# Kernel tuning notes

Hardware: AMD Instinct MI355X
Metric: run time of the kernel (lower is better)

## Reference

```python
import jax, jax.numpy as jnp
import numpy as np

B, S, D = 4, 2048, 1024

def setup_inputs() -> dict:
    key = jax.random.key(0)
    ks = jax.random.split(key, 4)
    scale = 1.0 / np.sqrt(D)
    return {
        "x": jax.random.normal(ks[0], (B, S, D), dtype=jnp.float32),
        "Wq": jax.random.normal(ks[1], (D, D), dtype=jnp.float32) * scale,
        "bq": jnp.zeros((D,), dtype=jnp.float32),
        "Wk": jax.random.normal(ks[2], (D, D), dtype=jnp.float32) * scale,
        "bk": jnp.zeros((D,), dtype=jnp.float32),
        "Wv": jax.random.normal(ks[3], (D, D), dtype=jnp.float32) * scale,
        "bv": jnp.zeros((D,), dtype=jnp.float32),
    }

def reference(x, Wq, bq, Wk, bk, Wv, bv):
    d = x.shape[-1]
    Q = jnp.einsum('bsd,df->bsf', x, Wq) + bq  # [B,S,D]
    K = jnp.einsum('bsd,df->bsf', x, Wk) + bk
    V = jnp.einsum('bsd,df->bsf', x, Wv) + bv
    scores = jnp.einsum('bqd,bkd->bqk', Q, K) / jnp.sqrt(jnp.asarray(d, x.dtype))  # [B,S,S]
    weights = jax.nn.softmax(scores, axis=-1)
    return jnp.einsum('bqk,bkd->bqd', weights, V)  # [B,S,D]
```

## Files before the change

kernel.cpp:

```cpp
#include <hip/hip_runtime.h>
#include <stdint.h>


typedef __attribute__((ext_vector_type(8))) short bf16x8;
typedef __attribute__((ext_vector_type(4))) float f32x4;
typedef __attribute__((ext_vector_type(4))) unsigned short u16x4;
typedef __attribute__((ext_vector_type(8))) unsigned short u16x8;

__device__ __forceinline__ unsigned short f2bf(float f) {
  union { float f; unsigned u; } v; v.f = f;
  return (unsigned short)((v.u + 0x7FFFu + ((v.u >> 16) & 1u)) >> 16);
}
__device__ __forceinline__ unsigned short f2h(float f) {
  union { _Float16 h; unsigned short u; } v; v.h = (_Float16)f;
  return v.u;
}
__device__ __forceinline__ float h2f(unsigned short u) {
  union { unsigned short u; _Float16 h; } v; v.u = u;
  return (float)v.h;
}

__device__ __forceinline__ void gload16(const void* g, void* l) {
  __builtin_amdgcn_global_load_lds(
      (const __attribute__((address_space(1))) unsigned int*)g,
      (__attribute__((address_space(3))) unsigned int*)l, 16, 0, 0);
}

template <int N>
__device__ __forceinline__ void wait_vm() {
  asm volatile("s_waitcnt vmcnt(%0)" ::"n"(N) : "memory");
}

__device__ __forceinline__ int swz8(int bid, int cpx) {
  return (bid & 7) * cpx + (bid >> 3);
}

__device__ __forceinline__ f32x4 mfma16(bf16x8 a, bf16x8 b, f32x4 c) {
  return __builtin_amdgcn_mfma_f32_16x16x32_bf16(a, b, c, 0, 0, 0);
}

__device__ __forceinline__ void gemm_core(
    const unsigned short* __restrict__ A, const unsigned short* __restrict__ Bt,
    const int lda, const int ldb, const int nt,
    const long aRow0, const long bRow0, char* lds,
    f32x4 (&acc)[8][4]) {
  constexpr int A_BYTES = 256 * 64;
  constexpr int SLOT = A_BYTES + 128 * 64;
  constexpr int LA = 4, LB = 2, L = LA + LB;
  const int tid = threadIdx.x;
  const int lane = tid & 63;
  const int wid = tid >> 6;
  const int wm = wid >> 1, wn = wid & 1;
  const int l15 = lane & 15, lhi = lane >> 4;

  long goffA[LA]; int ldsoffA[LA];
#pragma unroll
  for (int j = 0; j < LA; ++j) {
    const int local = j * 4096 + tid * 16;
    const int row = local >> 6, ch = (local >> 4) & 3;
    goffA[j] = (aRow0 + row) * (long)lda + ((ch ^ ((row >> 1) & 3)) << 3);
    ldsoffA[j] = local;
  }
  long goffB[LB]; int ldsoffB[LB];
#pragma unroll
  for (int j = 0; j < LB; ++j) {
    const int local = j * 4096 + tid * 16;
    const int row = local >> 6, ch = (local >> 4) & 3;
    goffB[j] = (bRow0 + row) * (long)ldb + ((ch ^ ((row >> 1) & 3)) << 3);
    ldsoffB[j] = A_BYTES + local;
  }
  int raddrA[8];
#pragma unroll
  for (int m = 0; m < 8; ++m) {
    const int row = wm * 128 + m * 16 + l15;
    raddrA[m] = row * 64 + ((lhi ^ ((row >> 1) & 3)) << 4);
  }
  int raddrB[4];
#pragma unroll
  for (int n = 0; n < 4; ++n) {
    const int row = wn * 64 + n * 16 + l15;
    raddrB[n] = A_BYTES + row * 64 + ((lhi ^ ((row >> 1) & 3)) << 4);
  }

  const f32x4 z4 = {0.f, 0.f, 0.f, 0.f};
#pragma unroll
  for (int m = 0; m < 8; ++m)
#pragma unroll
    for (int n = 0; n < 4; ++n) acc[m][n] = z4;

  auto stage_tile = [&](int T) {
    char* dst = lds + (T % 3) * SLOT;
    const int k0 = T << 5;
#pragma unroll
    for (int j = 0; j < LA; ++j) gload16(A + goffA[j] + k0, dst + ldsoffA[j]);
#pragma unroll
    for (int j = 0; j < LB; ++j) gload16(Bt + goffB[j] + k0, dst + ldsoffB[j]);
  };

  stage_tile(0);
  stage_tile(1);
  wait_vm<L>();
  __builtin_amdgcn_s_barrier();

  for (int t = 0; t < nt; ++t) {
    const char* sb = lds + (t % 3) * SLOT;
    bf16x8 af[8], bfr[4];
#pragma unroll
    for (int n = 0; n < 4; ++n) bfr[n] = *(const bf16x8*)(sb + raddrB[n]);
#pragma unroll
    for (int m = 0; m < 8; ++m) af[m] = *(const bf16x8*)(sb + raddrA[m]);
    if (t + 2 < nt) stage_tile(t + 2);
    __builtin_amdgcn_s_setprio(1);
#pragma unroll
    for (int m = 0; m < 8; ++m)
#pragma unroll
      for (int n = 0; n < 4; ++n) acc[m][n] = mfma16(af[m], bfr[n], acc[m][n]);
    __builtin_amdgcn_s_setprio(0);
    if (t + 2 < nt) wait_vm<L>();
    else if (t + 1 < nt) wait_vm<0>();
    __builtin_amdgcn_s_barrier();
  }
}

__global__ __launch_bounds__(256, 2) void qkv_kernel(
    const unsigned short* __restrict__ X, const unsigned short* __restrict__ TQ,
    const unsigned short* __restrict__ TK, const unsigned short* __restrict__ TV,
    const float* __restrict__ bq, const float* __restrict__ bk,
    const float* __restrict__ bv, unsigned short* __restrict__ Q16,
    unsigned short* __restrict__ K16, unsigned short* __restrict__ VT) {
  __shared__ char lds[3 * 24576];
  const int wgid = swz8(blockIdx.x, 96);
  const int tm = wgid / 24, tn = wgid % 24;
  const int w = tn >> 3, c = tn & 7;
  const unsigned short* Bt = w == 0 ? TQ : (w == 1 ? TK : TV);
  const float* bias = w == 0 ? bq : (w == 1 ? bk : bv);

  f32x4 acc[8][4];
  gemm_core(X, Bt, 1024, 1024, 32, (long)tm * 256, (long)c * 128, lds, acc);

  const int tid = threadIdx.x, lane = tid & 63, wid = tid >> 6;
  const int wm = wid >> 1, wn = wid & 1;
  const int l15 = lane & 15, lhi = lane >> 4;
  const int rowBase = tm * 256 + wm * 128;
  const int colBase = c * 128 + wn * 64;
  if (w < 2) {
    unsigned short* C = w == 0 ? Q16 : K16;
#pragma unroll
    for (int m = 0; m < 8; ++m)
#pragma unroll
      for (int n = 0; n < 4; ++n) {
        const int col = colBase + n * 16 + l15;
        const float bvv = bias[col];
#pragma unroll
        for (int j = 0; j < 4; ++j) {
          const int row = rowBase + m * 16 + lhi * 4 + j;
          C[(long)row * 1024 + col] = f2bf(acc[m][n][j] + bvv);
        }
      }
  } else {
#pragma unroll
    for (int m = 0; m < 8; ++m)
#pragma unroll
      for (int n = 0; n < 4; ++n) {
        const int col = colBase + n * 16 + l15;
        const float bvv = bias[col];
        const int row0 = rowBase + m * 16 + lhi * 4;
        const int b = row0 >> 11, s = row0 & 2047;
        u16x4 v;
#pragma unroll
        for (int j = 0; j < 4; ++j) v[j] = f2bf(acc[m][n][j] + bvv);
        *reinterpret_cast<u16x4*>(&VT[(long)b * 2097152 + (long)col * 2048 + s]) = v;
      }
  }
}

__global__ __launch_bounds__(256, 2) void scores_kernel(
    const unsigned short* __restrict__ Q16, const unsigned short* __restrict__ K16,
    unsigned short* __restrict__ SC16) {
  __shared__ char lds[3 * 24576];
  const int wgid = swz8(blockIdx.x, 64);
  const int bz = wgid >> 7, tm = (wgid >> 4) & 7, tn = wgid & 15;
  const unsigned short* A = Q16 + (long)bz * 2097152;
  const unsigned short* Bt = K16 + (long)bz * 2097152;

  f32x4 acc[8][4];
  gemm_core(A, Bt, 1024, 1024, 32, (long)tm * 256, (long)tn * 128, lds, acc);

  unsigned short* C = SC16 + (long)bz * 4194304;
  const int tid = threadIdx.x, lane = tid & 63, wid = tid >> 6;
  const int wm = wid >> 1, wn = wid & 1;
  const int l15 = lane & 15, lhi = lane >> 4;
  const int rowBase = tm * 256 + wm * 128;
  const int colBase = tn * 128 + wn * 64;
#pragma unroll
  for (int m = 0; m < 8; ++m)
#pragma unroll
    for (int n = 0; n < 4; ++n) {
      const int col = colBase + n * 16 + l15;
#pragma unroll
      for (int j = 0; j < 4; ++j) {
        const int row = rowBase + m * 16 + lhi * 4 + j;
        C[(long)row * 2048 + col] = f2h(acc[m][n][j] * (1.f / 32.f));
      }
    }
}

__global__ __launch_bounds__(256, 2) void pv_kernel(
    const unsigned short* __restrict__ P16, const unsigned short* __restrict__ VT,
    float* __restrict__ out) {
  __shared__ char lds[3 * 24576];
  const int wgid = swz8(blockIdx.x, 32);
  const int bz = wgid >> 6, tm = (wgid >> 3) & 7, tn = wgid & 7;
  const unsigned short* A = P16 + (long)bz * 4194304;
  const unsigned short* Bt = VT + (long)bz * 2097152;

  f32x4 acc[8][4];
  gemm_core(A, Bt, 2048, 2048, 64, (long)tm * 256, (long)tn * 128, lds, acc);

  float* C = out + (long)bz * 2097152;
  const int tid = threadIdx.x, lane = tid & 63, wid = tid >> 6;
  const int wm = wid >> 1, wn = wid & 1;
  const int l15 = lane & 15, lhi = lane >> 4;
  const int rowBase = tm * 256 + wm * 128;
  const int colBase = tn * 128 + wn * 64;
#pragma unroll
  for (int m = 0; m < 8; ++m)
#pragma unroll
    for (int n = 0; n < 4; ++n) {
      const int col = colBase + n * 16 + l15;
#pragma unroll
      for (int j = 0; j < 4; ++j) {
        const int row = rowBase + m * 16 + lhi * 4 + j;
        C[(long)row * 1024 + col] = acc[m][n][j];
      }
    }
}

__global__ __launch_bounds__(256) void cvt4(const float* __restrict__ in,
                                            unsigned short* __restrict__ out) {
  int i = blockIdx.x * 256 + threadIdx.x;
  float4 v = reinterpret_cast<const float4*>(in)[i];
  u16x4 r;
  r[0] = f2bf(v.x); r[1] = f2bf(v.y); r[2] = f2bf(v.z); r[3] = f2bf(v.w);
  reinterpret_cast<u16x4*>(out)[i] = r;
}

__global__ __launch_bounds__(256) void cvtWt(
    const float* __restrict__ w0, const float* __restrict__ w1, const float* __restrict__ w2,
    unsigned short* __restrict__ t0, unsigned short* __restrict__ t1, unsigned short* __restrict__ t2) {
  const float* w = blockIdx.y == 0 ? w0 : (blockIdx.y == 1 ? w1 : w2);
  unsigned short* t = blockIdx.y == 0 ? t0 : (blockIdx.y == 1 ? t1 : t2);
  int id = blockIdx.x * 256 + threadIdx.x;
  int k = id >> 10, n = id & 1023;
  t[n * 1024 + k] = f2bf(w[id]);
}

__global__ __launch_bounds__(256) void softmax_rows(const unsigned short* __restrict__ S,
                                                    unsigned short* __restrict__ P) {
  const long row = blockIdx.x;
  const u16x8* src = reinterpret_cast<const u16x8*>(S + row * 2048);
  const int tid = threadIdx.x;
  u16x8 a = src[tid];
  float v[8];
#pragma unroll
  for (int i = 0; i < 8; ++i) v[i] = h2f(a[i]);
  float m = v[0];
#pragma unroll
  for (int i = 1; i < 8; ++i) m = fmaxf(m, v[i]);
#pragma unroll
  for (int o = 32; o > 0; o >>= 1) m = fmaxf(m, __shfl_xor(m, o));
  __shared__ float red[8];
  const int wid = tid >> 6, lane = tid & 63;
  if (lane == 0) red[wid] = m;
  __syncthreads();
  m = fmaxf(fmaxf(red[0], red[1]), fmaxf(red[2], red[3]));
  float s = 0.f;
#pragma unroll
  for (int i = 0; i < 8; ++i) { v[i] = __expf(v[i] - m); s += v[i]; }
#pragma unroll
  for (int o = 32; o > 0; o >>= 1) s += __shfl_xor(s, o);
  if (lane == 0) red[4 + wid] = s;
  __syncthreads();
  s = (red[4] + red[5]) + (red[6] + red[7]);
  const float inv = 1.f / s;
  u16x8 p;
#pragma unroll
  for (int i = 0; i < 8; ++i) p[i] = f2bf(v[i] * inv);
  reinterpret_cast<u16x8*>(P + row * 2048)[tid] = p;
}

extern "C" void kernel_launch(void* const* d_in, const int* in_sizes, int n_in,
                              void* d_out, int out_size, void* d_ws, size_t ws_size,
                              hipStream_t stream) {
  const float* x  = (const float*)d_in[0];
  const float* Wq = (const float*)d_in[1];
  const float* bq = (const float*)d_in[2];
  const float* Wk = (const float*)d_in[3];
  const float* bk = (const float*)d_in[4];
  const float* Wv = (const float*)d_in[5];
  const float* bv = (const float*)d_in[6];
  float* out = (float*)d_out;

  char* ws = (char*)d_ws;
  const size_t MB = 1024 * 1024;
  unsigned short* X16 = (unsigned short*)(ws);
  unsigned short* TQ  = (unsigned short*)(ws + 16 * MB);
  unsigned short* TK  = (unsigned short*)(ws + 18 * MB);
  unsigned short* TV  = (unsigned short*)(ws + 20 * MB);
  unsigned short* Q16 = (unsigned short*)(ws + 22 * MB);
  unsigned short* K16 = (unsigned short*)(ws + 38 * MB);
  unsigned short* VT  = (unsigned short*)(ws + 54 * MB);
  unsigned short* SC16 = (unsigned short*)(ws + 70 * MB);
  unsigned short* P16 = Q16;

  cvt4<<<8192, 256, 0, stream>>>(x, X16);
  cvtWt<<<dim3(4096, 3), 256, 0, stream>>>(Wq, Wk, Wv, TQ, TK, TV);

  qkv_kernel<<<768, 256, 0, stream>>>(X16, TQ, TK, TV, bq, bk, bv, Q16, K16, VT);
  scores_kernel<<<512, 256, 0, stream>>>(Q16, K16, SC16);
  softmax_rows<<<4 * 2048, 256, 0, stream>>>(SC16, P16);
  pv_kernel<<<256, 256, 0, stream>>>(P16, VT, out);

  (void)in_sizes; (void)n_in; (void)out_size; (void)ws_size;
}
```

Before: 176.2 us.

## Use 256x256 tiles with 8-wave workgroups and split-phase GEMM pipeline

```diff
diff --git a/kernel.cpp b/kernel.cpp
--- a/kernel.cpp
+++ b/kernel.cpp
@@ -37,6 +37,108 @@
 
 __device__ __forceinline__ f32x4 mfma16(bf16x8 a, bf16x8 b, f32x4 c) {
   return __builtin_amdgcn_mfma_f32_16x16x32_bf16(a, b, c, 0, 0, 0);
+}
+
+__device__ __forceinline__ void gemm_core2(
+    const unsigned short* __restrict__ A, const unsigned short* __restrict__ Bt,
+    const int lda, const int ldb, const int nt,
+    const long aRow0, const long bRow0, char* lds,
+    f32x4 (&acc)[8][4]) {
+  constexpr int A_BYTES = 256 * 64;
+  constexpr int SLOT = 2 * A_BYTES;
+  const int tid = threadIdx.x;
+  const int lane = tid & 63;
+  const int wid = tid >> 6;
+  const int wm = wid >> 2, wn = wid & 3;
+  const int l15 = lane & 15, lhi = lane >> 4;
+
+  long goffA[2]; int ldsoffA[2];
+#pragma unroll
+  for (int j = 0; j < 2; ++j) {
+    const int local = j * 8192 + tid * 16;
+    const int row = local >> 6, ch = (local >> 4) & 3;
+    goffA[j] = (aRow0 + row) * (long)lda + ((ch ^ ((row >> 1) & 3)) << 3);
+    ldsoffA[j] = local;
+  }
+  long goffB[2]; int ldsoffB[2];
+#pragma unroll
+  for (int j = 0; j < 2; ++j) {
+    const int local = j * 8192 + tid * 16;
+    const int row = local >> 6, ch = (local >> 4) & 3;
+    goffB[j] = (bRow0 + row) * (long)ldb + ((ch ^ ((row >> 1) & 3)) << 3);
+    ldsoffB[j] = A_BYTES + local;
+  }
+  int raddrA[8];
+#pragma unroll
+  for (int m = 0; m < 8; ++m) {
+    const int row = wm * 128 + m * 16 + l15;
+    raddrA[m] = row * 64 + ((lhi ^ ((row >> 1) & 3)) << 4);
+  }
+  int raddrB[4];
+#pragma unroll
+  for (int n = 0; n < 4; ++n) {
+    const int row = wn * 64 + n * 16 + l15;
+    raddrB[n] = A_BYTES + row * 64 + ((lhi ^ ((row >> 1) & 3)) << 4);
+  }
+
+  const f32x4 z4 = {0.f, 0.f, 0.f, 0.f};
+#pragma unroll
+  for (int m = 0; m < 8; ++m)
+#pragma unroll
+    for (int n = 0; n < 4; ++n) acc[m][n] = z4;
+
+  auto stage_A = [&](int T) {
+    char* dst = lds + (T % 3) * SLOT;
+    const int k0 = T << 5;
+#pragma unroll
+    for (int j = 0; j < 2; ++j) gload16(A + goffA[j] + k0, dst + ldsoffA[j]);
+  };
+  auto stage_B = [&](int T) {
+    char* dst = lds + (T % 3) * SLOT;
+    const int k0 = T << 5;
+#pragma unroll
+    for (int j = 0; j < 2; ++j) gload16(Bt + goffB[j] + k0, dst + ldsoffB[j]);
+  };
+
+  stage_A(0); stage_B(0);
+  stage_A(1); stage_B(1);
+  wait_vm<4>();
+  __builtin_amdgcn_s_barrier();
+
+  for (int t = 0; t < nt; ++t) {
+    const char* sb = lds + (t % 3) * SLOT;
+    bf16x8 af[4], af2[4], bfr[4];
+#pragma unroll
+    for (int n = 0; n < 4; ++n) bfr[n] = *(const bf16x8*)(sb + raddrB[n]);
+#pragma unroll
+    for (int m = 0; m < 4; ++m) af[m] = *(const bf16x8*)(sb + raddrA[m]);
+    if (t + 2 < nt) stage_A(t + 2);
+    __builtin_amdgcn_s_barrier();
+    __builtin_amdgcn_s_setprio(1);
+#pragma unroll
+    for (int m = 0; m < 4; ++m)
+#pragma unroll
+      for (int n = 0; n < 4; ++n) acc[m][n] = mfma16(af[m], bfr[n], acc[m][n]);
+    __builtin_amdgcn_s_setprio(0);
+    __builtin_amdgcn_s_barrier();
+#pragma unroll
+    for (int m = 0; m < 4; ++m) af2[m] = *(const bf16x8*)(sb + raddrA[4 + m]);
+    if (t + 2 < nt) {
+      stage_B(t + 2);
+      wait_vm<4>();
+    } else if (t + 1 < nt) {
+      wait_vm<0>();
+    }
+    __builtin_amdgcn_s_barrier();
+    __builtin_amdgcn_s_setprio(1);
+#pragma unroll
+    for (int m = 0; m < 4; ++m)
+#pragma unroll
+      for (int n = 0; n < 4; ++n)
+        acc[4 + m][n] = mfma16(af2[m], bfr[n], acc[4 + m][n]);
+    __builtin_amdgcn_s_setprio(0);
+    __builtin_amdgcn_s_barrier();
+  }
 }
 
 __device__ __forceinline__ void gemm_core(
@@ -122,27 +224,27 @@
   }
 }
 
-__global__ __launch_bounds__(256, 2) void qkv_kernel(
+__global__ __launch_bounds__(512, 2) void qkv_kernel(
     const unsigned short* __restrict__ X, const unsigned short* __restrict__ TQ,
     const unsigned short* __restrict__ TK, const unsigned short* __restrict__ TV,
     const float* __restrict__ bq, const float* __restrict__ bk,
     const float* __restrict__ bv, unsigned short* __restrict__ Q16,
     unsigned short* __restrict__ K16, unsigned short* __restrict__ VT) {
-  __shared__ char lds[3 * 24576];
-  const int wgid = swz8(blockIdx.x, 96);
-  const int tm = wgid / 24, tn = wgid % 24;
-  const int w = tn >> 3, c = tn & 7;
+  __shared__ char lds[3 * 32768];
+  const int wgid = swz8(blockIdx.x, 48);
+  const int tm = wgid / 12, tn = wgid % 12;
+  const int w = tn >> 2, c = tn & 3;
   const unsigned short* Bt = w == 0 ? TQ : (w == 1 ? TK : TV);
   const float* bias = w == 0 ? bq : (w == 1 ? bk : bv);
 
   f32x4 acc[8][4];
-  gemm_core(X, Bt, 1024, 1024, 32, (long)tm * 256, (long)c * 128, lds, acc);
+  gemm_core2(X, Bt, 1024, 1024, 32, (long)tm * 256, (long)c * 256, lds, acc);
 
   const int tid = threadIdx.x, lane = tid & 63, wid = tid >> 6;
-  const int wm = wid >> 1, wn = wid & 1;
+  const int wm = wid >> 2, wn = wid & 3;
   const int l15 = lane & 15, lhi = lane >> 4;
   const int rowBase = tm * 256 + wm * 128;
-  const int colBase = c * 128 + wn * 64;
+  const int colBase = c * 256 + wn * 64;
   if (w < 2) {
     unsigned short* C = w == 0 ? Q16 : K16;
 #pragma unroll
@@ -174,24 +276,24 @@
   }
 }
 
-__global__ __launch_bounds__(256, 2) void scores_kernel(
+__global__ __launch_bounds__(512, 2) void scores_kernel(
     const unsigned short* __restrict__ Q16, const unsigned short* __restrict__ K16,
     unsigned short* __restrict__ SC16) {
-  __shared__ char lds[3 * 24576];
-  const int wgid = swz8(blockIdx.x, 64);
-  const int bz = wgid >> 7, tm = (wgid >> 4) & 7, tn = wgid & 15;
+  __shared__ char lds[3 * 32768];
+  const int wgid = swz8(blockIdx.x, 32);
+  const int bz = wgid >> 6, tm = (wgid >> 3) & 7, tn = wgid & 7;
   const unsigned short* A = Q16 + (long)bz * 2097152;
   const unsigned short* Bt = K16 + (long)bz * 2097152;
 
   f32x4 acc[8][4];
-  gemm_core(A, Bt, 1024, 1024, 32, (long)tm * 256, (long)tn * 128, lds, acc);
+  gemm_core2(A, Bt, 1024, 1024, 32, (long)tm * 256, (long)tn * 256, lds, acc);
 
   unsigned short* C = SC16 + (long)bz * 4194304;
   const int tid = threadIdx.x, lane = tid & 63, wid = tid >> 6;
-  const int wm = wid >> 1, wn = wid & 1;
+  const int wm = wid >> 2, wn = wid & 3;
   const int l15 = lane & 15, lhi = lane >> 4;
   const int rowBase = tm * 256 + wm * 128;
-  const int colBase = tn * 128 + wn * 64;
+  const int colBase = tn * 256 + wn * 64;
 #pragma unroll
   for (int m = 0; m < 8; ++m)
 #pragma unroll
@@ -316,8 +418,8 @@
   cvt4<<<8192, 256, 0, stream>>>(x, X16);
   cvtWt<<<dim3(4096, 3), 256, 0, stream>>>(Wq, Wk, Wv, TQ, TK, TV);
 
-  qkv_kernel<<<768, 256, 0, stream>>>(X16, TQ, TK, TV, bq, bk, bv, Q16, K16, VT);
-  scores_kernel<<<512, 256, 0, stream>>>(Q16, K16, SC16);
+  qkv_kernel<<<384, 512, 0, stream>>>(X16, TQ, TK, TV, bq, bk, bv, Q16, K16, VT);
+  scores_kernel<<<256, 512, 0, stream>>>(Q16, K16, SC16);
   softmax_rows<<<4 * 2048, 256, 0, stream>>>(SC16, P16);
   pv_kernel<<<256, 256, 0, stream>>>(P16, VT, out);
 
```

Measured after the change: 185.6 us. 5.3% more time.
